# Kernel tuning notes

Measured on AMD Instinct MI355X. Metric: run time of the kernel, lower is better.

Reference implementation:

```python
import jax, jax.numpy as jnp
import numpy as np

N, E, D, H, C = 100000, 1600000, 128, 256, 40


def setup_inputs() -> dict:
    key = jax.random.key(0)
    ks = jax.random.split(key, 10)
    x = jax.random.normal(ks[0], (N, D), dtype=jnp.float32)
    src = jax.random.randint(ks[1], (E,), 0, N, dtype=jnp.int32)
    dst = jax.random.randint(ks[2], (E,), 0, N, dtype=jnp.int32)
    # GIN layer 1 MLP (bias-free), kaiming-uniform-like scale 1/sqrt(fan_in)
    w1a = jax.random.normal(ks[3], (D, H), dtype=jnp.float32) / np.sqrt(D)
    w1b = jax.random.normal(ks[4], (H, H), dtype=jnp.float32) / np.sqrt(H)
    # GIN layer 2 MLP
    w2a = jax.random.normal(ks[5], (H, H), dtype=jnp.float32) / np.sqrt(H)
    w2b = jax.random.normal(ks[6], (H, H), dtype=jnp.float32) / np.sqrt(H)
    # eps initialized to 0 per reset_parameters
    eps1 = jnp.zeros((), dtype=jnp.float32)
    eps2 = jnp.zeros((), dtype=jnp.float32)
    # final classifier fc (with bias)
    fc_w = jax.random.normal(ks[7], (H, C), dtype=jnp.float32) / np.sqrt(H)
    fc_b = jax.random.normal(ks[8], (C,), dtype=jnp.float32) * 0.01
    return {"x": x, "src": src, "dst": dst,
            "eps1": eps1, "w1a": w1a, "w1b": w1b,
            "eps2": eps2, "w2a": w2a, "w2b": w2b,
            "fc_w": fc_w, "fc_b": fc_b}


def reference(x, src, dst, eps1, w1a, w1b, eps2, w2a, w2b, fc_w, fc_b):
    n = x.shape[0]

    def gin_layer(h, eps, wa, wb):
        # GINConv sum-aggregation: scatter-add neighbor feats over edges
        agg = jax.ops.segment_sum(h[src], dst, num_segments=n)  # [N, d]
        rst = (1.0 + eps) * h + agg
        # 2-layer bias-free MLP with ReLU between
        return jax.nn.relu(rst @ wa) @ wb

    h = jax.nn.relu(gin_layer(x, eps1, w1a, w1b))   # layer + outer activation
    h = jax.nn.relu(gin_layer(h, eps2, w2a, w2b))   # dropout p=0 -> identity
    return h @ fc_w + fc_b                           # [N, C]
```

## Files before the change

### kernel.cpp

```cpp
#include <hip/hip_runtime.h>

#define N_NODES 100000
#define N_EDGES 1600000
#define DIM_IN  128
#define DIM_H   256
#define DIM_C   40

#define NB   391
#define NBLK 391
#define CHUNK 4096
#define ECAP 6144

typedef unsigned short bf16_t;
typedef __attribute__((ext_vector_type(8))) short short8;
typedef __attribute__((ext_vector_type(4))) float f32x4;

__device__ __forceinline__ bf16_t f2b(float f) {
    unsigned int u = __float_as_uint(f);
    unsigned int r = (u + 0x7fffu + ((u >> 16) & 1u)) >> 16;
    return (bf16_t)r;
}

__device__ __forceinline__ void gl_lds16(const void* gsrc, void* ldst) {
    __builtin_amdgcn_global_load_lds(
        (const __attribute__((address_space(1))) void*)gsrc,
        (__attribute__((address_space(3))) void*)ldst,
        16, 0, 0);
}


__global__ void k_bhist(const int* __restrict__ dst, int* __restrict__ cnt2, int e) {
    __shared__ int h[NB];
    int t = threadIdx.x, blk = blockIdx.x;
    for (int i = t; i < NB; i += 256) h[i] = 0;
    __syncthreads();
    int base = blk * CHUNK;
    int end = min(base + CHUNK, e);
    for (int i = base + t; i < end; i += 256)
        atomicAdd(&h[dst[i] >> 8], 1);
    __syncthreads();
    for (int i = t; i < NB; i += 256) cnt2[blk * NB + i] = h[i];
}

__global__ void k_bscanA(const int* __restrict__ cnt2, int* __restrict__ basep,
                         int* __restrict__ btot) {
    __shared__ int s[512];
    int t = threadIdx.x, b = blockIdx.x;
    int v = (t < NBLK) ? cnt2[t * NB + b] : 0;
    s[t] = v;
    __syncthreads();
    #pragma unroll
    for (int d = 1; d < 512; d <<= 1) {
        int tv = (t >= d) ? s[t - d] : 0;
        __syncthreads();
        s[t] += tv;
        __syncthreads();
    }
    if (t < NBLK) basep[t * NB + b] = s[t] - v;
    if (t == 511) btot[b] = s[511];
}

__global__ void k_bscan2(const int* __restrict__ btot, int* __restrict__ boff) {
    __shared__ int s[512];
    int t = threadIdx.x;
    int v = (t < NB) ? btot[t] : 0;
    s[t] = v;
    __syncthreads();
    #pragma unroll
    for (int d = 1; d < 512; d <<= 1) {
        int tv = (t >= d) ? s[t - d] : 0;
        __syncthreads();
        s[t] += tv;
        __syncthreads();
    }
    if (t < NB) boff[t] = s[t] - v;
    if (t == NB - 1) boff[NB] = s[t];
}

__global__ void k_bscatter(const int* __restrict__ src, const int* __restrict__ dst,
                           const int* __restrict__ basep, const int* __restrict__ boff,
                           int* __restrict__ ebuf, int e) {
    __shared__ int cur[NB];
    int t = threadIdx.x, blk = blockIdx.x;
    for (int i = t; i < NB; i += 256) cur[i] = basep[blk * NB + i] + boff[i];
    __syncthreads();
    int base = blk * CHUNK;
    int end = min(base + CHUNK, e);
    for (int i = base + t; i < end; i += 256) {
        int sv = src[i], dv = dst[i];
        int pos = atomicAdd(&cur[dv >> 8], 1);
        ebuf[pos] = sv | ((dv & 255) << 24);
    }
}

__global__ __launch_bounds__(256) void k_build(const int* __restrict__ ebuf,
                                               const int* __restrict__ boff,
                                               int* __restrict__ off,
                                               int* __restrict__ csr) {
    __shared__ int ec[ECAP];
    __shared__ int h[256];
    __shared__ int cur[256];
    int t = threadIdx.x, b = blockIdx.x;
    int node0 = b << 8;
    int e0 = boff[b], e1 = boff[b + 1];
    int ne = e1 - e0;
    bool fits = (ne <= ECAP);
    h[t] = 0;
    __syncthreads();
    if (fits) {
        for (int i = t; i < ne; i += 256) {
            int p = ebuf[e0 + i];
            ec[i] = p;
            atomicAdd(&h[(unsigned)p >> 24], 1);
        }
    } else {
        for (int i = t; i < ne; i += 256)
            atomicAdd(&h[(unsigned)ebuf[e0 + i] >> 24], 1);
    }
    __syncthreads();
    int mydeg = h[t];
    #pragma unroll
    for (int d = 1; d < 256; d <<= 1) {
        int tv = (t >= d) ? h[t - d] : 0;
        __syncthreads();
        h[t] += tv;
        __syncthreads();
    }
    int node = node0 + t;
    if (node < N_NODES) off[node + 1] = e0 + h[t];
    if (b == 0 && t == 0) off[0] = 0;
    cur[t] = e0 + h[t] - mydeg;
    __syncthreads();
    if (fits) {
        for (int i = t; i < ne; i += 256) {
            int p = ec[i];
            int pos = atomicAdd(&cur[(unsigned)p >> 24], 1);
            csr[pos] = p & 0xFFFFFF;
        }
    } else {
        for (int i = t; i < ne; i += 256) {
            int p = ebuf[e0 + i];
            int pos = atomicAdd(&cur[(unsigned)p >> 24], 1);
            csr[pos] = p & 0xFFFFFF;
        }
    }
}


__global__ void k_cvt_i8(const float* __restrict__ x, signed char* __restrict__ x8,
                         float* __restrict__ xs, int n) {
    int gid = blockIdx.x * blockDim.x + threadIdx.x;
    int u = gid >> 6, lane = gid & 63;
    if (u >= n) return;
    float2 v = *(const float2*)(x + (size_t)u * 128 + lane * 2);
    float m = fmaxf(fabsf(v.x), fabsf(v.y));
    #pragma unroll
    for (int d = 1; d < 64; d <<= 1)
        m = fmaxf(m, __shfl_xor(m, d, 64));
    float inv = (m > 0.f) ? 127.f / m : 0.f;
    int q0 = (int)rintf(v.x * inv);
    int q1 = (int)rintf(v.y * inv);
    unsigned short pk = (unsigned short)((q0 & 0xff) | ((q1 & 0xff) << 8));
    *(unsigned short*)(x8 + ((unsigned)u << 7) + lane * 2) = pk;
    if (lane == 0) xs[u] = (m > 0.f) ? m * (1.f / 127.f) : 0.f;
}

__global__ void k_wcvt(const float* __restrict__ w1a, const float* __restrict__ w1b,
                       const float* __restrict__ w2a, const float* __restrict__ w2b,
                       const float* __restrict__ fcw,
                       bf16_t* __restrict__ o1a, bf16_t* __restrict__ o1b,
                       bf16_t* __restrict__ o2a, bf16_t* __restrict__ o2b,
                       bf16_t* __restrict__ ofc) {
    int r = blockIdx.y;
    int idx = blockIdx.x * 256 + threadIdx.x;
    const float* in; bf16_t* out; int K, N, Npad;
    switch (r) {
        case 0: in = w1a; out = o1a; K = 128; N = 256; Npad = 256; break;
        case 1: in = w1b; out = o1b; K = 256; N = 256; Npad = 256; break;
        case 2: in = w2a; out = o2a; K = 256; N = 256; Npad = 256; break;
        case 3: in = w2b; out = o2b; K = 256; N = 256; Npad = 256; break;
        default: in = fcw; out = ofc; K = 256; N = 40;  Npad = 128; break;
    }
    if (idx >= Npad * K) return;
    int n = idx / K, k = idx - n * K;
    float v = (n < N) ? in[(size_t)k * N + n] : 0.f;
    out[idx] = f2b(v);
}


__global__ void k_agg_i8(const signed char* __restrict__ h8, const float* __restrict__ hs,
                         const int* __restrict__ off, const int* __restrict__ csr,
                         const float* __restrict__ eps_p,
                         bf16_t* __restrict__ rst, int n) {
    int gid = blockIdx.x * blockDim.x + threadIdx.x;
    int u = __builtin_amdgcn_readfirstlane(gid >> 6);
    int lane = threadIdx.x & 63;
    if (u >= n) return;

    float acc0 = 0.f, acc1 = 0.f;
    int r0 = off[u], r1 = off[u + 1];
    unsigned loff = lane * 2u;

    for (int base = r0; base < r1; base += 64) {
        int m = r1 - base; if (m > 64) m = 64;
        int li = (lane < m) ? lane : (m - 1);
        int iv = csr[base + li];
        for (int c = 0; c < m; c += 16) {
            int s[16]; float sc[16]; unsigned v[16];
            #pragma unroll
            for (int t = 0; t < 16; t++)
                s[t] = __builtin_amdgcn_readlane(iv, c + t);
            #pragma unroll
            for (int t = 0; t < 16; t++)
                sc[t] = (c + t < m) ? hs[s[t]] : 0.f;
            #pragma unroll
            for (int t = 0; t < 16; t++)
                v[t] = *(const unsigned short*)(h8 + (((unsigned)s[t] << 7) + loff));
            #pragma unroll
            for (int t = 0; t < 16; t++) {
                acc0 += (float)(int)(signed char)(v[t] & 0xffu) * sc[t];
                acc1 += (float)(int)(signed char)(v[t] >> 8) * sc[t];
            }
        }
    }

    float scu = hs[u] * (1.0f + eps_p[0]);
    unsigned vu = *(const unsigned short*)(h8 + (((unsigned)u << 7) + loff));
    float o0 = (float)(int)(signed char)(vu & 0xffu) * scu + acc0;
    float o1 = (float)(int)(signed char)(vu >> 8) * scu + acc1;
    *(unsigned int*)(rst + ((unsigned)u << 7) + lane * 2) =
        (unsigned int)f2b(o0) | ((unsigned int)f2b(o1) << 16);
}


__global__ void k_agg_u8(const unsigned char* __restrict__ h8,
                         const float* __restrict__ hs,
                         const int* __restrict__ off, const int* __restrict__ csr,
                         const float* __restrict__ eps_p,
                         bf16_t* __restrict__ rst, int n) {
    int gid = blockIdx.x * blockDim.x + threadIdx.x;
    int u = __builtin_amdgcn_readfirstlane(gid >> 6);
    int lane = threadIdx.x & 63;
    if (u >= n) return;

    float acc[4] = {0.f, 0.f, 0.f, 0.f};
    int r0 = off[u], r1 = off[u + 1];
    unsigned loff = lane * 4u;

    for (int base = r0; base < r1; base += 64) {
        int m = r1 - base; if (m > 64) m = 64;
        int li = (lane < m) ? lane : (m - 1);
        int iv = csr[base + li];
        for (int c = 0; c < m; c += 16) {
            int s[16]; float sc[16]; unsigned int v[16];
            #pragma unroll
            for (int t = 0; t < 16; t++)
                s[t] = __builtin_amdgcn_readlane(iv, c + t);
            #pragma unroll
            for (int t = 0; t < 16; t++)
                sc[t] = (c + t < m) ? hs[s[t]] : 0.f;
            #pragma unroll
            for (int t = 0; t < 16; t++)
                v[t] = *(const unsigned int*)(h8 + (((unsigned)s[t] << 8) + loff));
            #pragma unroll
            for (int t = 0; t < 16; t++) {
                acc[0] += (float)(v[t] & 0xffu) * sc[t];
                acc[1] += (float)((v[t] >> 8) & 0xffu) * sc[t];
                acc[2] += (float)((v[t] >> 16) & 0xffu) * sc[t];
                acc[3] += (float)(v[t] >> 24) * sc[t];
            }
        }
    }

    float ep = 1.0f + eps_p[0];
    unsigned int vu = *(const unsigned int*)(h8 + (((unsigned)u << 8) + loff));
    float scu = hs[u] * ep;
    float o0 = (float)(vu & 0xffu) * scu + acc[0];
    float o1 = (float)((vu >> 8) & 0xffu) * scu + acc[1];
    float o2 = (float)((vu >> 16) & 0xffu) * scu + acc[2];
    float o3 = (float)(vu >> 24) * scu + acc[3];
    uint2 ov;
    ov.x = (unsigned int)f2b(o0) | ((unsigned int)f2b(o1) << 16);
    ov.y = (unsigned int)f2b(o2) | ((unsigned int)f2b(o3) << 16);
    *(uint2*)(rst + (size_t)u * 256 + lane * 4) = ov;
}


#define TS_STRIDE 264

template <int K1, bool OUT8, bool FUSE_FC>
__global__ __launch_bounds__(256, 2) void k_mlp(
    const bf16_t* __restrict__ A, const bf16_t* __restrict__ W1t,
    const bf16_t* __restrict__ W2t, bf16_t* __restrict__ H,
    unsigned char* __restrict__ H8, float* __restrict__ Hs,
    const bf16_t* __restrict__ FCt, const float* __restrict__ fc_b,
    float* __restrict__ Cout, int M)
{
    __shared__ __align__(16) bf16_t As[64 * 32];
    __shared__ __align__(16) bf16_t Bs[256 * 32];
    __shared__ __align__(16) bf16_t Ts[64 * TS_STRIDE];
    __shared__ int rmax[64];

    int tid = threadIdx.x;
    int wave = tid >> 6, lane = tid & 63;
    int l15 = lane & 15, quad = lane >> 4;
    int bm = blockIdx.x * 64;
    int wn = wave * 64;

    f32x4 acc[4][4];
    #pragma unroll
    for (int i = 0; i < 4; i++)
        #pragma unroll
        for (int j = 0; j < 4; j++) acc[i][j] = 0.f;

    for (int k0 = 0; k0 < K1; k0 += 32) {
        {
            int row = tid >> 2, k8 = (tid & 3) * 8;
            int gr = bm + row; if (gr >= M) gr = M - 1;
            gl_lds16(A + (size_t)gr * K1 + k0 + k8, &As[(wave * 64) * 8]);
        }
        #pragma unroll
        for (int l = 0; l < 4; l++) {
            int s = l * 256 + tid;
            int row = s >> 2, k8 = (s & 3) * 8;
            gl_lds16(W1t + (size_t)row * K1 + k0 + k8, &Bs[(size_t)(l * 256 + wave * 64) * 8]);
        }
        __syncthreads();

        short8 af[4], bfv[4];
        #pragma unroll
        for (int i = 0; i < 4; i++)
            af[i] = *(const short8*)&As[(i * 16 + l15) * 32 + quad * 8];
        #pragma unroll
        for (int j = 0; j < 4; j++)
            bfv[j] = *(const short8*)&Bs[(wn + j * 16 + l15) * 32 + quad * 8];

        #pragma unroll
        for (int i = 0; i < 4; i++)
            #pragma unroll
            for (int j = 0; j < 4; j++)
                acc[i][j] = __builtin_amdgcn_mfma_f32_16x16x32_bf16(af[i], bfv[j], acc[i][j], 0, 0, 0);
        __syncthreads();
    }

    #pragma unroll
    for (int i = 0; i < 4; i++)
        #pragma unroll
        for (int j = 0; j < 4; j++) {
            int row = i * 16 + quad * 4;
            int col = wn + j * 16 + l15;
            #pragma unroll
            for (int r = 0; r < 4; r++)
                Ts[(row + r) * TS_STRIDE + col] = f2b(fmaxf(acc[i][j][r], 0.f));
        }

    #pragma unroll
    for (int i = 0; i < 4; i++)
        #pragma unroll
        for (int j = 0; j < 4; j++) acc[i][j] = 0.f;
    __syncthreads();

    for (int k0 = 0; k0 < 256; k0 += 32) {
        #pragma unroll
        for (int l = 0; l < 4; l++) {
            int s = l * 256 + tid;
            int row = s >> 2, k8 = (s & 3) * 8;
            gl_lds16(W2t + (size_t)row * 256 + k0 + k8, &Bs[(size_t)(l * 256 + wave * 64) * 8]);
        }
        __syncthreads();

        short8 af[4], bfv[4];
        #pragma unroll
        for (int i = 0; i < 4; i++)
            af[i] = *(const short8*)&Ts[(i * 16 + l15) * TS_STRIDE + k0 + quad * 8];
        #pragma unroll
        for (int j = 0; j < 4; j++)
            bfv[j] = *(const short8*)&Bs[(wn + j * 16 + l15) * 32 + quad * 8];

        #pragma unroll
        for (int i = 0; i < 4; i++)
            #pragma unroll
            for (int j = 0; j < 4; j++)
                acc[i][j] = __builtin_amdgcn_mfma_f32_16x16x32_bf16(af[i], bfv[j], acc[i][j], 0, 0, 0);
        __syncthreads();
    }

    if constexpr (OUT8) {
        if (tid < 64) rmax[tid] = 0;
        __syncthreads();
        #pragma unroll
        for (int i = 0; i < 4; i++)
            #pragma unroll
            for (int r = 0; r < 4; r++) {
                float m = 0.f;
                #pragma unroll
                for (int j = 0; j < 4; j++) m = fmaxf(m, acc[i][j][r]);
                atomicMax(&rmax[i * 16 + quad * 4 + r], __float_as_int(m));
            }
        __syncthreads();
        #pragma unroll
        for (int i = 0; i < 4; i++) {
            #pragma unroll
            for (int r = 0; r < 4; r++) {
                int row = i * 16 + quad * 4 + r;
                int rowg = bm + row;
                if (rowg >= M) continue;
                float rm = __int_as_float(rmax[row]);
                float inv = (rm > 0.f) ? 255.f / rm : 0.f;
                #pragma unroll
                for (int j = 0; j < 4; j++) {
                    int col = wn + j * 16 + l15;
                    float v = fmaxf(acc[i][j][r], 0.f);
                    unsigned q = (unsigned)(v * inv + 0.5f);
                    if (q > 255u) q = 255u;
                    H8[(size_t)rowg * 256 + col] = (unsigned char)q;
                }
                if (wave == 0 && l15 == 0)
                    Hs[rowg] = rm * (1.f / 255.f);
            }
        }
    } else if constexpr (FUSE_FC) {
        #pragma unroll
        for (int i = 0; i < 4; i++)
            #pragma unroll
            for (int j = 0; j < 4; j++) {
                int row = i * 16 + quad * 4;
                int col = wn + j * 16 + l15;
                #pragma unroll
                for (int r = 0; r < 4; r++)
                    Ts[(row + r) * TS_STRIDE + col] = f2b(fmaxf(acc[i][j][r], 0.f));
            }
        __syncthreads();

        f32x4 acc3[3];
        #pragma unroll
        for (int j = 0; j < 3; j++) acc3[j] = 0.f;

        for (int k0 = 0; k0 < 256; k0 += 32) {
            {
                int row = tid >> 2, k8 = (tid & 3) * 8;
                gl_lds16(FCt + (size_t)row * 256 + k0 + k8, &Bs[(wave * 64) * 8]);
            }
            __syncthreads();

            short8 af = *(const short8*)&Ts[(wave * 16 + l15) * TS_STRIDE + k0 + quad * 8];
            #pragma unroll
            for (int j = 0; j < 3; j++) {
                short8 bfv = *(const short8*)&Bs[(j * 16 + l15) * 32 + quad * 8];
                acc3[j] = __builtin_amdgcn_mfma_f32_16x16x32_bf16(af, bfv, acc3[j], 0, 0, 0);
            }
            __syncthreads();
        }

        #pragma unroll
        for (int j = 0; j < 3; j++) {
            int col = j * 16 + l15;
            if (col >= DIM_C) continue;
            float bv = fc_b[col];
            #pragma unroll
            for (int r = 0; r < 4; r++) {
                int rowg = bm + wave * 16 + quad * 4 + r;
                if (rowg < M)
                    Cout[(size_t)rowg * DIM_C + col] = acc3[j][r] + bv;
            }
        }
    } else {
        #pragma unroll
        for (int j = 0; j < 4; j++) {
            int col = wn + j * 16 + l15;
            #pragma unroll
            for (int i = 0; i < 4; i++) {
                #pragma unroll
                for (int r = 0; r < 4; r++) {
                    int rowg = bm + i * 16 + quad * 4 + r;
                    if (rowg < M)
                        H[(size_t)rowg * 256 + col] = f2b(fmaxf(acc[i][j][r], 0.f));
                }
            }
        }
    }
}


static inline size_t rnd256(size_t x) { return (x + 255) & ~(size_t)255; }

extern "C" void kernel_launch(void* const* d_in, const int* in_sizes, int n_in,
                              void* d_out, int out_size, void* d_ws, size_t ws_size,
                              hipStream_t stream) {
    const float* x    = (const float*)d_in[0];
    const int*   src  = (const int*)d_in[1];
    const int*   dst  = (const int*)d_in[2];
    const float* eps1 = (const float*)d_in[3];
    const float* w1a  = (const float*)d_in[4];
    const float* w1b  = (const float*)d_in[5];
    const float* eps2 = (const float*)d_in[6];
    const float* w2a  = (const float*)d_in[7];
    const float* w2b  = (const float*)d_in[8];
    const float* fc_w = (const float*)d_in[9];
    const float* fc_b = (const float*)d_in[10];
    float* out = (float*)d_out;

    char* w = (char*)d_ws;
    int* off  = (int*)w; w += rnd256(sizeof(int) * (size_t)(N_NODES + 1));
    int* csr  = (int*)w; w += rnd256(sizeof(int) * (size_t)N_EDGES);
    int* cnt2  = (int*)w; w += rnd256(sizeof(int) * (size_t)NBLK * NB);
    int* basep = (int*)w; w += rnd256(sizeof(int) * (size_t)NBLK * NB);
    int* btot  = (int*)w; w += rnd256(sizeof(int) * 512);
    int* boff  = (int*)w; w += rnd256(sizeof(int) * (NB + 1));
    bf16_t* w1a_t = (bf16_t*)w; w += rnd256(2 * (size_t)DIM_H * DIM_IN);
    bf16_t* w1b_t = (bf16_t*)w; w += rnd256(2 * (size_t)DIM_H * DIM_H);
    bf16_t* w2a_t = (bf16_t*)w; w += rnd256(2 * (size_t)DIM_H * DIM_H);
    bf16_t* w2b_t = (bf16_t*)w; w += rnd256(2 * (size_t)DIM_H * DIM_H);
    bf16_t* fc_t  = (bf16_t*)w; w += rnd256(2 * (size_t)128 * DIM_H);
    signed char* x8 = (signed char*)w; w += rnd256((size_t)N_NODES * DIM_IN);
    float* xs = (float*)w; w += rnd256(sizeof(float) * (size_t)N_NODES);
    unsigned char* h8 = (unsigned char*)w; w += rnd256((size_t)N_NODES * DIM_H);
    float* hs = (float*)w; w += rnd256(sizeof(float) * (size_t)N_NODES);
    bf16_t* R12 = (bf16_t*)w; w += rnd256(2 * (size_t)N_NODES * DIM_H);
    bf16_t* R3  = (bf16_t*)w; w += rnd256(2 * (size_t)N_NODES * DIM_H);

    bf16_t* rst1 = R12;
    int* ebuf = (int*)R3;

    k_bhist<<<NBLK, 256, 0, stream>>>(dst, cnt2, N_EDGES);
    k_bscanA<<<NB, 512, 0, stream>>>(cnt2, basep, btot);
    k_bscan2<<<1, 512, 0, stream>>>(btot, boff);
    k_bscatter<<<NBLK, 256, 0, stream>>>(src, dst, basep, boff, ebuf, N_EDGES);
    k_build<<<NB, 256, 0, stream>>>(ebuf, boff, off, csr);

    k_cvt_i8<<<(N_NODES * 64 + 255) / 256, 256, 0, stream>>>(x, x8, xs, N_NODES);
    {
        dim3 g(256, 5);
        k_wcvt<<<g, 256, 0, stream>>>(w1a, w1b, w2a, w2b, fc_w,
                                      w1a_t, w1b_t, w2a_t, w2b_t, fc_t);
    }

    const int agg_blocks = (N_NODES * 64 + 255) / 256;
    const int mlp_blocks = (N_NODES + 63) / 64;

    k_agg_i8<<<agg_blocks, 256, 0, stream>>>(x8, xs, off, csr, eps1, rst1, N_NODES);
    k_mlp<DIM_IN, true, false><<<mlp_blocks, 256, 0, stream>>>(
        rst1, w1a_t, w1b_t, nullptr, h8, hs, nullptr, nullptr, nullptr, N_NODES);

    k_agg_u8<<<agg_blocks, 256, 0, stream>>>(h8, hs, off, csr, eps2, (bf16_t*)R3, N_NODES);
    k_mlp<DIM_H, false, true><<<mlp_blocks, 256, 0, stream>>>(
        (bf16_t*)R3, w2a_t, w2b_t, nullptr, nullptr, nullptr, fc_t, fc_b, out, N_NODES);
}
```

Baseline: 417.1 us.

## Double-buffer LDS tiles in fused MLP kernel to overlap loads with MFMA

Converts the three k-loops of the fused MLP kernel (first GEMM, second GEMM, fused FC) to double-buffered shared-memory staging. The next tile is issued via global_load_lds before computing on the current one, with explicit vmcnt waits and raw barriers replacing __syncthreads. This aims to hide global load latency behind MFMA work. It doubles the As/Bs shared memory, which may reduce occupancy at 2 blocks per CU, and relies on hand-counted vmcnt values being correct.

New measurement: 410.5 us. About the same (-1.6%).

```diff
diff --git a/kernel.cpp b/kernel.cpp
--- a/kernel.cpp
+++ b/kernel.cpp
@@ -296,8 +296,8 @@
     const bf16_t* __restrict__ FCt, const float* __restrict__ fc_b,
     float* __restrict__ Cout, int M)
 {
-    __shared__ __align__(16) bf16_t As[64 * 32];
-    __shared__ __align__(16) bf16_t Bs[256 * 32];
+    __shared__ __align__(16) bf16_t As[2][64 * 32];
+    __shared__ __align__(16) bf16_t Bs[2][256 * 32];
     __shared__ __align__(16) bf16_t Ts[64 * TS_STRIDE];
     __shared__ int rmax[64];
 
@@ -307,40 +307,64 @@
     int bm = blockIdx.x * 64;
     int wn = wave * 64;
 
-    f32x4 acc[4][4];
-    #pragma unroll
-    for (int i = 0; i < 4; i++)
-        #pragma unroll
-        for (int j = 0; j < 4; j++) acc[i][j] = 0.f;
-
-    for (int k0 = 0; k0 < K1; k0 += 32) {
+    auto stage1 = [&](int k0, int b) {
         {
             int row = tid >> 2, k8 = (tid & 3) * 8;
             int gr = bm + row; if (gr >= M) gr = M - 1;
-            gl_lds16(A + (size_t)gr * K1 + k0 + k8, &As[(wave * 64) * 8]);
+            gl_lds16(A + (size_t)gr * K1 + k0 + k8, &As[b][(wave * 64) * 8]);
         }
         #pragma unroll
         for (int l = 0; l < 4; l++) {
             int s = l * 256 + tid;
             int row = s >> 2, k8 = (s & 3) * 8;
-            gl_lds16(W1t + (size_t)row * K1 + k0 + k8, &Bs[(size_t)(l * 256 + wave * 64) * 8]);
-        }
-        __syncthreads();
+            gl_lds16(W1t + (size_t)row * K1 + k0 + k8, &Bs[b][(size_t)(l * 256 + wave * 64) * 8]);
+        }
+    };
+    auto stage2 = [&](int k0, int b) {
+        #pragma unroll
+        for (int l = 0; l < 4; l++) {
+            int s = l * 256 + tid;
+            int row = s >> 2, k8 = (s & 3) * 8;
+            gl_lds16(W2t + (size_t)row * 256 + k0 + k8, &Bs[b][(size_t)(l * 256 + wave * 64) * 8]);
+        }
+    };
+
+    f32x4 acc[4][4];
+    #pragma unroll
+    for (int i = 0; i < 4; i++)
+        #pragma unroll
+        for (int j = 0; j < 4; j++) acc[i][j] = 0.f;
+
+    constexpr int NS1 = K1 / 32;
+    stage1(0, 0);
+    for (int k = 0; k < NS1; k++) {
+        int cur = k & 1;
+        if (k + 1 < NS1) {
+            stage1((k + 1) * 32, cur ^ 1);
+            asm volatile("s_waitcnt vmcnt(5)" ::: "memory");
+        } else {
+            asm volatile("s_waitcnt vmcnt(0)" ::: "memory");
+        }
+        __builtin_amdgcn_sched_barrier(0);
+        __builtin_amdgcn_s_barrier();
 
         short8 af[4], bfv[4];
         #pragma unroll
         for (int i = 0; i < 4; i++)
-            af[i] = *(const short8*)&As[(i * 16 + l15) * 32 + quad * 8];
+            af[i] = *(const short8*)&As[cur][(i * 16 + l15) * 32 + quad * 8];
         #pragma unroll
         for (int j = 0; j < 4; j++)
-            bfv[j] = *(const short8*)&Bs[(wn + j * 16 + l15) * 32 + quad * 8];
+            bfv[j] = *(const short8*)&Bs[cur][(wn + j * 16 + l15) * 32 + quad * 8];
 
         #pragma unroll
         for (int i = 0; i < 4; i++)
             #pragma unroll
             for (int j = 0; j < 4; j++)
                 acc[i][j] = __builtin_amdgcn_mfma_f32_16x16x32_bf16(af[i], bfv[j], acc[i][j], 0, 0, 0);
-        __syncthreads();
+
+        asm volatile("s_waitcnt lgkmcnt(0)" ::: "memory");
+        __builtin_amdgcn_sched_barrier(0);
+        __builtin_amdgcn_s_barrier();
     }
 
     #pragma unroll
@@ -360,29 +384,35 @@
         for (int j = 0; j < 4; j++) acc[i][j] = 0.f;
     __syncthreads();
 
-    for (int k0 = 0; k0 < 256; k0 += 32) {
-        #pragma unroll
-        for (int l = 0; l < 4; l++) {
-            int s = l * 256 + tid;
-            int row = s >> 2, k8 = (s & 3) * 8;
-            gl_lds16(W2t + (size_t)row * 256 + k0 + k8, &Bs[(size_t)(l * 256 + wave * 64) * 8]);
-        }
-        __syncthreads();
+    stage2(0, 0);
+    for (int k = 0; k < 8; k++) {
+        int cur = k & 1;
+        if (k + 1 < 8) {
+            stage2((k + 1) * 32, cur ^ 1);
+            asm volatile("s_waitcnt vmcnt(4)" ::: "memory");
+        } else {
+            asm volatile("s_waitcnt vmcnt(0)" ::: "memory");
+        }
+        __builtin_amdgcn_sched_barrier(0);
+        __builtin_amdgcn_s_barrier();
 
         short8 af[4], bfv[4];
         #pragma unroll
         for (int i = 0; i < 4; i++)
-            af[i] = *(const short8*)&Ts[(i * 16 + l15) * TS_STRIDE + k0 + quad * 8];
+            af[i] = *(const short8*)&Ts[(i * 16 + l15) * TS_STRIDE + k * 32 + quad * 8];
         #pragma unroll
         for (int j = 0; j < 4; j++)
-            bfv[j] = *(const short8*)&Bs[(wn + j * 16 + l15) * 32 + quad * 8];
+            bfv[j] = *(const short8*)&Bs[cur][(wn + j * 16 + l15) * 32 + quad * 8];
 
         #pragma unroll
         for (int i = 0; i < 4; i++)
             #pragma unroll
             for (int j = 0; j < 4; j++)
                 acc[i][j] = __builtin_amdgcn_mfma_f32_16x16x32_bf16(af[i], bfv[j], acc[i][j], 0, 0, 0);
-        __syncthreads();
+
+        asm volatile("s_waitcnt lgkmcnt(0)" ::: "memory");
+        __builtin_amdgcn_sched_barrier(0);
+        __builtin_amdgcn_s_barrier();
     }
 
     if constexpr (OUT8) {
@@ -436,20 +466,33 @@
         #pragma unroll
         for (int j = 0; j < 3; j++) acc3[j] = 0.f;
 
-        for (int k0 = 0; k0 < 256; k0 += 32) {
-            {
-                int row = tid >> 2, k8 = (tid & 3) * 8;
-                gl_lds16(FCt + (size_t)row * 256 + k0 + k8, &Bs[(wave * 64) * 8]);
-            }
-            __syncthreads();
-
-            short8 af = *(const short8*)&Ts[(wave * 16 + l15) * TS_STRIDE + k0 + quad * 8];
+        auto stage3 = [&](int k0, int b) {
+            int row = tid >> 2, k8 = (tid & 3) * 8;
+            gl_lds16(FCt + (size_t)row * 256 + k0 + k8, &Bs[b][(wave * 64) * 8]);
+        };
+
+        stage3(0, 0);
+        for (int k = 0; k < 8; k++) {
+            int cur = k & 1;
+            if (k + 1 < 8) {
+                stage3((k + 1) * 32, cur ^ 1);
+                asm volatile("s_waitcnt vmcnt(1)" ::: "memory");
+            } else {
+                asm volatile("s_waitcnt vmcnt(0)" ::: "memory");
+            }
+            __builtin_amdgcn_sched_barrier(0);
+            __builtin_amdgcn_s_barrier();
+
+            short8 af = *(const short8*)&Ts[(wave * 16 + l15) * TS_STRIDE + k * 32 + quad * 8];
             #pragma unroll
             for (int j = 0; j < 3; j++) {
-                short8 bfv = *(const short8*)&Bs[(j * 16 + l15) * 32 + quad * 8];
+                short8 bfv = *(const short8*)&Bs[cur][(j * 16 + l15) * 32 + quad * 8];
                 acc3[j] = __builtin_amdgcn_mfma_f32_16x16x32_bf16(af, bfv, acc3[j], 0, 0, 0);
             }
-            __syncthreads();
+
+            asm volatile("s_waitcnt lgkmcnt(0)" ::: "memory");
+            __builtin_amdgcn_sched_barrier(0);
+            __builtin_amdgcn_s_barrier();
         }
 
         #pragma unroll
```
